# Optimization experiments

Hardware: AMD Instinct MI355X
Metric: run time of the kernel (lower is better)

Reference implementation:

```python
import jax, jax.numpy as jnp
import numpy as np

N = 400000   # active voxels
C = 64       # channels
G = 128      # voxel grid side
K = 27       # 3x3x3 kernel offsets
EPS = 1e-5   # BatchNorm eps


def _build_kernel_maps(rng):
    # random sparse 3D coordinates (unique voxels in a G^3 grid)
    lin = rng.choice(G ** 3, size=N, replace=False)
    coords = np.stack(np.unravel_index(lin, (G, G, G)), -1).astype(np.int64)  # [N,3]
    lut = np.full(G ** 3, N, dtype=np.int32)  # sentinel N = missing neighbor
    lut[lin] = np.arange(N, dtype=np.int32)
    offs = np.stack(np.meshgrid([-1, 0, 1], [-1, 0, 1], [-1, 0, 1], indexing='ij'), -1).reshape(-1, 3)  # [27,3]
    nbr = np.full((3, K, N), N, dtype=np.int32)
    for di, d in enumerate((1, 2, 3)):
        for k in range(K):
            nc = coords + offs[k] * d
            valid = np.all((nc >= 0) & (nc < G), axis=1)
            idx = np.ravel_multi_index(nc[valid].T, (G, G, G))
            nbr[di, k, valid] = lut[idx]
    return nbr


def setup_inputs() -> dict:
    key = jax.random.key(0)
    ks = jax.random.split(key, 20)
    rng = np.random.default_rng(0)
    nbr = jnp.asarray(_build_kernel_maps(rng))  # [3,27,N] int32
    s = 0.05
    inp = {
        'feats': jax.random.normal(ks[0], (N, C), jnp.float32),
        'nbr': nbr,
        # conv_init (dilation 1) + its BN
        'W_init': jax.random.normal(ks[1], (K, C, C), jnp.float32) * s,
        'b_init': jax.random.normal(ks[2], (C,), jnp.float32) * s,
        'g_init': jnp.ones((C,), jnp.float32),
        'be_init': jnp.zeros((C,), jnp.float32),
        'm_init': jax.random.normal(ks[3], (C,), jnp.float32) * s,
        'v_init': jax.random.uniform(ks[4], (C,), jnp.float32, 0.5, 1.5),
        # three branches (dilations 1,2,3), stacked on leading axis
        'W_br': jax.random.normal(ks[5], (3, K, C, C), jnp.float32) * s,
        'b_br': jax.random.normal(ks[6], (3, C), jnp.float32) * s,
        'g_br': jnp.ones((3, C), jnp.float32),
        'be_br': jnp.zeros((3, C), jnp.float32),
        'm_br': jax.random.normal(ks[7], (3, C), jnp.float32) * s,
        'v_br': jax.random.uniform(ks[8], (3, C), jnp.float32, 0.5, 1.5),
        # conv_out: 1x1 conv C -> 1
        'W_out': jax.random.normal(ks[9], (C, 1), jnp.float32) * s,
        'b_out': jax.random.normal(ks[10], (1,), jnp.float32) * s,
    }
    return inp


def _sparse_conv3(feats, nbr_k, W, b):
    # feats [N,C], nbr_k [27,N] (index N = missing), W [27,C,Cout], b [Cout]
    fpad = jnp.concatenate([feats, jnp.zeros((1, feats.shape[1]), feats.dtype)], 0)
    def step(acc, wn):
        Wk, nk = wn
        return acc + fpad[nk] @ Wk, None
    init = jnp.zeros((feats.shape[0], W.shape[-1]), feats.dtype) + b
    out, _ = jax.lax.scan(step, init, (W, nbr_k))
    return out


def _bn_relu(x, g, b, m, v):
    # inference-mode BatchNorm followed by ReLU
    return jax.nn.relu((x - m) * (g * jax.lax.rsqrt(v + EPS)) + b)


def reference(feats, nbr, W_init, b_init, g_init, be_init, m_init, v_init,
              W_br, b_br, g_br, be_br, m_br, v_br, W_out, b_out):
    x_init = _bn_relu(_sparse_conv3(feats, nbr[0], W_init, b_init),
                      g_init, be_init, m_init, v_init)
    def branch(W, b, g, be, m, v, nb):
        return _bn_relu(_sparse_conv3(x_init, nb, W, b), g, be, m, v)
    xb = jax.vmap(branch)(W_br, b_br, g_br, be_br, m_br, v_br, nbr)  # [3,N,C]
    x_fused = xb.sum(0) + x_init
    att = jax.nn.sigmoid(x_fused @ W_out + b_out)  # [N,1]
    return att
```

## Files before the change

kernel.cpp:

```cpp
#include <hip/hip_runtime.h>
#include <hip/hip_bf16.h>
#include <math.h>

#define NV 400000
#define ROWS_BLK 192
#define GRID_CONV 2084

typedef __bf16 bfv8 __attribute__((ext_vector_type(8)));
typedef float f32x4 __attribute__((ext_vector_type(4)));

#define GLOAD_LDS16(gp, lp) __builtin_amdgcn_global_load_lds(                 \
    (const __attribute__((address_space(1))) void*)(gp),                     \
    (__attribute__((address_space(3))) void*)(lp), 16, 0, 0)

__global__ void prep_feats_k(const float* __restrict__ feats,
                             __bf16* __restrict__ fpad,
                             __bf16* __restrict__ xpad)
{
    long t = (long)blockIdx.x * blockDim.x + threadIdx.x;
    long base = t * 4;
    const long nfeat = (long)NV * 64;
    const long total = (long)(NV + 1) * 64;
    if (base < total) {
        float x0 = 0.f, x1 = 0.f, x2 = 0.f, x3 = 0.f;
        if (base < nfeat) {
            const float4 v = *(const float4*)(feats + base);
            x0 = v.x; x1 = v.y; x2 = v.z; x3 = v.w;
        }
        union { __bf16 b[4]; ushort4 u; } pk;
        pk.b[0] = (__bf16)x0; pk.b[1] = (__bf16)x1;
        pk.b[2] = (__bf16)x2; pk.b[3] = (__bf16)x3;
        *(ushort4*)(fpad + base) = pk.u;
    }
    if (t < 64) xpad[(long)NV * 64 + t] = (__bf16)0.f;
}

__global__ void prep_w_k(const float* __restrict__ Winit,
                         const float* __restrict__ Wbr,
                         __bf16* __restrict__ wpk)
{
    int e = blockIdx.x * 256 + threadIdx.x;
    int i  = e & 7;
    int l  = (e >> 3) & 63;
    int cb = (e >> 9) & 3;
    int kc = (e >> 11) & 1;
    int kk = e >> 12;
    int k  = kk % 27;
    int s  = kk / 27;
    int cin  = kc * 32 + (l >> 4) * 8 + i;
    int cout = cb * 16 + (l & 15);
    float v = (s == 0) ? Winit[(k * 64 + cin) * 64 + cout]
                       : Wbr[(((s - 1) * 27 + k) * 64 + cin) * 64 + cout];
    wpk[e] = (__bf16)v;
}

__global__ void prep_bn_k(const float* __restrict__ b_init, const float* __restrict__ g_init,
                          const float* __restrict__ be_init, const float* __restrict__ m_init,
                          const float* __restrict__ v_init,
                          const float* __restrict__ b_br, const float* __restrict__ g_br,
                          const float* __restrict__ be_br, const float* __restrict__ m_br,
                          const float* __restrict__ v_br,
                          float* __restrict__ scale, float* __restrict__ shiftb)
{
    int t = threadIdx.x;
    int s = t >> 6, c = t & 63;
    float g, be, m, v, b;
    if (s == 0) { g = g_init[c]; be = be_init[c]; m = m_init[c]; v = v_init[c]; b = b_init[c]; }
    else { int o = (s - 1) * 64 + c; g = g_br[o]; be = be_br[o]; m = m_br[o]; v = v_br[o]; b = b_br[o]; }
    float sc = g / sqrtf(v + 1e-5f);
    scale[t]  = sc;
    shiftb[t] = (b - m) * sc + be;
}

struct Idx3 { int v[3]; };

__device__ __forceinline__ Idx3 load_idx3(const int* __restrict__ nbr_t,
                                          long base, int l15)
{
    Idx3 r;
#pragma unroll
    for (int rg = 0; rg < 3; rg++) {
        long rr = base + rg * 16 + l15;
        rr = (rr < NV) ? rr : (NV - 1);
        r.v[rg] = nbr_t[rr];
    }
    return r;
}

__device__ __forceinline__ void stage_b(const __bf16* __restrict__ wtap,
                                        __bf16* lds_dst, int wid, int lane)
{
#pragma unroll
    for (int j = 0; j < 2; j++) {
        int chunk = wid * 2 + j;
        const __bf16* gp = wtap + chunk * 512 + lane * 8;
        __bf16* lp = lds_dst + chunk * 512;
        GLOAD_LDS16(gp, lp);
    }
}

__device__ __forceinline__ void issue_A3(const __bf16* __restrict__ src,
                                         const Idx3 idx, int lg,
                                         bfv8 a0[3], bfv8 a1[3])
{
#pragma unroll
    for (int rg = 0; rg < 3; rg++) {
        const bfv8* ar = (const bfv8*)(src + (size_t)idx.v[rg] * 64);
        a0[rg] = ar[lg];
        a1[rg] = ar[4 + lg];
    }
}

__device__ __forceinline__ void mfma_tap3(const __bf16* bbuf, int lane,
                                          const bfv8 a0[3], const bfv8 a1[3],
                                          f32x4 acc[3][4])
{
    const bfv8* wp = (const bfv8*)bbuf;
#pragma unroll
    for (int cb = 0; cb < 4; cb++) {
        bfv8 b0 = wp[cb * 64 + lane];
#pragma unroll
        for (int rg = 0; rg < 3; rg++)
            acc[rg][cb] = __builtin_amdgcn_mfma_f32_16x16x32_bf16(a0[rg], b0, acc[rg][cb], 0, 0, 0);
    }
#pragma unroll
    for (int cb = 0; cb < 4; cb++) {
        bfv8 b1 = wp[(4 + cb) * 64 + lane];
#pragma unroll
        for (int rg = 0; rg < 3; rg++)
            acc[rg][cb] = __builtin_amdgcn_mfma_f32_16x16x32_bf16(a1[rg], b1, acc[rg][cb], 0, 0, 0);
    }
}


__global__ __launch_bounds__(256, 4)
void conv_init_k(const __bf16* __restrict__ fpad, const int* __restrict__ nbr,
                 const __bf16* __restrict__ wpk, const float* __restrict__ scale,
                 const float* __restrict__ shiftb, const float* __restrict__ wout,
                 __bf16* __restrict__ xpad, float* __restrict__ logitpart)
{
    __shared__ __bf16 smem[4 * 4096];
    __bf16* tile = smem;
    const int tid = threadIdx.x;
    const int wid = tid >> 6, lane = tid & 63;
    const int l15 = lane & 15, lg = lane >> 4;
    const long base = (long)blockIdx.x * ROWS_BLK + wid * 48;

    f32x4 acc[3][4];
    f32x4 z = {0.f, 0.f, 0.f, 0.f};
#pragma unroll
    for (int a = 0; a < 3; a++)
#pragma unroll
        for (int b = 0; b < 4; b++) acc[a][b] = z;

    stage_b(wpk,                    smem + 0 * 4096, wid, lane);
    stage_b(wpk + (size_t)1 * 4096, smem + 1 * 4096, wid, lane);
    Idx3 iA = load_idx3(nbr,                  base, l15);
    Idx3 iB = load_idx3(nbr + (size_t)1 * NV, base, l15);
    __syncthreads();

    bfv8 a0[3], a1[3];
    for (int k = 0; k < 27; k++) {
        issue_A3(fpad, iA, lg, a0, a1);
        int ts = (k + 2 < 27) ? (k + 2) : 26;
        stage_b(wpk + (size_t)ts * 4096, smem + ((k + 2) & 3) * 4096, wid, lane);
        Idx3 inew = load_idx3(nbr + (size_t)ts * NV, base, l15);
        __builtin_amdgcn_s_setprio(1);
        mfma_tap3(smem + (k & 3) * 4096, lane, a0, a1, acc);
        __builtin_amdgcn_s_setprio(0);
        iA = iB; iB = inew;
        asm volatile("s_waitcnt vmcnt(5)" ::: "memory");
        __builtin_amdgcn_s_barrier();
    }

    float sc[4], sh[4], wo[4];
#pragma unroll
    for (int cb = 0; cb < 4; cb++) {
        int col = cb * 16 + l15;
        sc[cb] = scale[col]; sh[cb] = shiftb[col]; wo[cb] = wout[col];
    }
    float lacc[3][4];
#pragma unroll
    for (int rg = 0; rg < 3; rg++)
#pragma unroll
        for (int j = 0; j < 4; j++) lacc[rg][j] = 0.f;

    __syncthreads();
#pragma unroll
    for (int rg = 0; rg < 3; rg++)
#pragma unroll
        for (int cb = 0; cb < 4; cb++)
#pragma unroll
            for (int j = 0; j < 4; j++) {
                float y = fmaxf(acc[rg][cb][j] * sc[cb] + sh[cb], 0.f);
                lacc[rg][j] += y * wo[cb];
                tile[(wid * 48 + rg * 16 + lg * 4 + j) * 64 + cb * 16 + l15] = (__bf16)y;
            }
    __syncthreads();

    for (int c = tid; c < 384; c += 256) {
        int r = c >> 1, h = c & 1;
        long grow = (long)blockIdx.x * ROWS_BLK + r;
        if (grow < NV) {
            const f32x4* srcp = (const f32x4*)(tile + r * 64 + h * 32);
            f32x4* dst = (f32x4*)(xpad + grow * 64 + h * 32);
#pragma unroll
            for (int q = 0; q < 4; q++) dst[q] = srcp[q];
        }
    }

#pragma unroll
    for (int rg = 0; rg < 3; rg++) {
        float red[4];
#pragma unroll
        for (int j = 0; j < 4; j++) {
            float t = lacc[rg][j];
            t += __shfl_xor(t, 1, 64);
            t += __shfl_xor(t, 2, 64);
            t += __shfl_xor(t, 4, 64);
            t += __shfl_xor(t, 8, 64);
            red[j] = t;
        }
        if (l15 == 0) {
            long row = base + rg * 16 + lg * 4;
            if (row < NV) {
                float4 o; o.x = red[0]; o.y = red[1]; o.z = red[2]; o.w = red[3];
                *(float4*)(logitpart + row) = o;
            }
        }
    }
}

__global__ __launch_bounds__(256, 4)
void conv_br_k(const __bf16* __restrict__ xpad, const int* __restrict__ nbr,
               const __bf16* __restrict__ wpk, const float* __restrict__ scale,
               const float* __restrict__ shiftb, const float* __restrict__ wout,
               const float* __restrict__ bout, const float* __restrict__ logitpart,
               float* __restrict__ att)
{
    __shared__ __bf16 bbuf[4][4096];
    const int tid = threadIdx.x;
    const int wid = tid >> 6, lane = tid & 63;
    const int l15 = lane & 15, lg = lane >> 4;
    const long base = (long)blockIdx.x * ROWS_BLK + wid * 48;

    float wo[4];
#pragma unroll
    for (int cb = 0; cb < 4; cb++) wo[cb] = wout[cb * 16 + l15];

    float lacc[3][4];
#pragma unroll
    for (int rg = 0; rg < 3; rg++)
#pragma unroll
        for (int j = 0; j < 4; j++) lacc[rg][j] = 0.f;

    f32x4 acc[3][4];
    f32x4 z = {0.f, 0.f, 0.f, 0.f};
#pragma unroll
    for (int a = 0; a < 3; a++)
#pragma unroll
        for (int b = 0; b < 4; b++) acc[a][b] = z;

    auto do_epi = [&](int d) {
        float sc[4], sh[4];
#pragma unroll
        for (int cb = 0; cb < 4; cb++) {
            int col = (d + 1) * 64 + cb * 16 + l15;
            sc[cb] = scale[col]; sh[cb] = shiftb[col];
        }
#pragma unroll
        for (int rg = 0; rg < 3; rg++)
#pragma unroll
            for (int cb = 0; cb < 4; cb++)
#pragma unroll
                for (int j = 0; j < 4; j++) {
                    float y = fmaxf(acc[rg][cb][j] * sc[cb] + sh[cb], 0.f);
                    lacc[rg][j] += y * wo[cb];
                }
#pragma unroll
        for (int a = 0; a < 3; a++)
#pragma unroll
            for (int b = 0; b < 4; b++) acc[a][b] = z;
    };

    stage_b(wpk + (size_t)27 * 4096, bbuf[0], wid, lane);
    stage_b(wpk + (size_t)28 * 4096, bbuf[1], wid, lane);
    Idx3 iA = load_idx3(nbr,                  base, l15);
    Idx3 iB = load_idx3(nbr + (size_t)1 * NV, base, l15);
    __syncthreads();

    bfv8 a0[3], a1[3];
    for (int k = 0; k < 81; k++) {
        issue_A3(xpad, iA, lg, a0, a1);
        int ts = (k + 2 < 81) ? (k + 2) : 80;
        stage_b(wpk + (size_t)(ts + 27) * 4096, bbuf[(k + 2) & 3], wid, lane);
        Idx3 inew = load_idx3(nbr + (size_t)ts * NV, base, l15);
        __builtin_amdgcn_s_setprio(1);
        mfma_tap3(bbuf[k & 3], lane, a0, a1, acc);
        __builtin_amdgcn_s_setprio(0);
        if (k == 26 || k == 53) do_epi(k / 27);
        iA = iB; iB = inew;
        asm volatile("s_waitcnt vmcnt(5)" ::: "memory");
        __builtin_amdgcn_s_barrier();
    }
    do_epi(2);

    float bo = bout[0];
#pragma unroll
    for (int rg = 0; rg < 3; rg++) {
        float red[4];
#pragma unroll
        for (int j = 0; j < 4; j++) {
            float t = lacc[rg][j];
            t += __shfl_xor(t, 1, 64);
            t += __shfl_xor(t, 2, 64);
            t += __shfl_xor(t, 4, 64);
            t += __shfl_xor(t, 8, 64);
            red[j] = t;
        }
        if (l15 == 0) {
            long row = base + rg * 16 + lg * 4;
            if (row < NV) {
                float4 lp = *(const float4*)(logitpart + row);
                float4 o;
                o.x = 1.f / (1.f + expf(-(red[0] + lp.x + bo)));
                o.y = 1.f / (1.f + expf(-(red[1] + lp.y + bo)));
                o.z = 1.f / (1.f + expf(-(red[2] + lp.z + bo)));
                o.w = 1.f / (1.f + expf(-(red[3] + lp.w + bo)));
                *(float4*)(att + row) = o;
            }
        }
    }
}

extern "C" void kernel_launch(void* const* d_in, const int* in_sizes, int n_in,
                              void* d_out, int out_size, void* d_ws, size_t ws_size,
                              hipStream_t stream)
{
    const float* feats  = (const float*)d_in[0];
    const int*   nbr    = (const int*)d_in[1];
    const float* W_init = (const float*)d_in[2];
    const float* b_init = (const float*)d_in[3];
    const float* g_init = (const float*)d_in[4];
    const float* be_init= (const float*)d_in[5];
    const float* m_init = (const float*)d_in[6];
    const float* v_init = (const float*)d_in[7];
    const float* W_br   = (const float*)d_in[8];
    const float* b_br   = (const float*)d_in[9];
    const float* g_br   = (const float*)d_in[10];
    const float* be_br  = (const float*)d_in[11];
    const float* m_br   = (const float*)d_in[12];
    const float* v_br   = (const float*)d_in[13];
    const float* W_out  = (const float*)d_in[14];
    const float* b_out  = (const float*)d_in[15];
    float* att = (float*)d_out;

    char* ws = (char*)d_ws;
    size_t off = 0;
    auto take = [&](size_t bytes) -> char* {
        char* p = ws + off;
        off = (off + bytes + 255) & ~(size_t)255;
        return p;
    };
    __bf16* fpad      = (__bf16*)take((size_t)(NV + 1) * 64 * 2);
    __bf16* xpad      = (__bf16*)take((size_t)(NV + 1) * 64 * 2);
    __bf16* wpk       = (__bf16*)take((size_t)4 * 27 * 4096 * 2);
    float*  scale     = (float*)take(4 * 64 * 4);
    float*  shiftb    = (float*)take(4 * 64 * 4);
    float*  logitpart = (float*)take((size_t)NV * 4);
    (void)in_sizes; (void)n_in; (void)out_size; (void)ws_size;

    prep_feats_k<<<25001, 256, 0, stream>>>(feats, fpad, xpad);
    prep_w_k<<<1728, 256, 0, stream>>>(W_init, W_br, wpk);
    prep_bn_k<<<1, 256, 0, stream>>>(b_init, g_init, be_init, m_init, v_init,
                                     b_br, g_br, be_br, m_br, v_br, scale, shiftb);
    conv_init_k<<<GRID_CONV, 256, 0, stream>>>(fpad, nbr, wpk, scale, shiftb,
                                               W_out, xpad, logitpart);
    conv_br_k<<<GRID_CONV, 256, 0, stream>>>(xpad, nbr, wpk, scale, shiftb,
                                             W_out, b_out, logitpart, att);
}
```

Measured before the change: 509.6 us.

## Double-buffer gathered A fragments one tap ahead in sparse conv kernels

Both conv kernels now prefetch the gathered feature rows for the next tap into a second register set while the MFMAs for the current tap run. Neighbor indices are loaded three taps ahead instead of two. The waitcnt and barrier move to before the MFMA so that only the current A and B data must have arrived. The extra registers lower launch_bounds occupancy from 4 to 3 blocks per SM, trading latency hiding through occupancy for latency hiding through software pipelining.

```diff
diff --git a/kernel.cpp b/kernel.cpp
--- a/kernel.cpp
+++ b/kernel.cpp
@@ -133,7 +133,7 @@
 }
 
 
-__global__ __launch_bounds__(256, 4)
+__global__ __launch_bounds__(256, 3)
 void conv_init_k(const __bf16* __restrict__ fpad, const int* __restrict__ nbr,
                  const __bf16* __restrict__ wpk, const float* __restrict__ scale,
                  const float* __restrict__ shiftb, const float* __restrict__ wout,
@@ -155,22 +155,28 @@
 
     stage_b(wpk,                    smem + 0 * 4096, wid, lane);
     stage_b(wpk + (size_t)1 * 4096, smem + 1 * 4096, wid, lane);
-    Idx3 iA = load_idx3(nbr,                  base, l15);
-    Idx3 iB = load_idx3(nbr + (size_t)1 * NV, base, l15);
+    Idx3 i0 = load_idx3(nbr,                  base, l15);
+    Idx3 i1 = load_idx3(nbr + (size_t)1 * NV, base, l15);
+    Idx3 i2 = load_idx3(nbr + (size_t)2 * NV, base, l15);
     __syncthreads();
 
-    bfv8 a0[3], a1[3];
+    bfv8 aC0[3], aC1[3], aN0[3], aN1[3];
+    issue_A3(fpad, i0, lg, aC0, aC1);
+
     for (int k = 0; k < 27; k++) {
-        issue_A3(fpad, iA, lg, a0, a1);
+        issue_A3(fpad, i1, lg, aN0, aN1);
         int ts = (k + 2 < 27) ? (k + 2) : 26;
         stage_b(wpk + (size_t)ts * 4096, smem + ((k + 2) & 3) * 4096, wid, lane);
-        Idx3 inew = load_idx3(nbr + (size_t)ts * NV, base, l15);
+        int tn = (k + 3 < 27) ? (k + 3) : 26;
+        Idx3 inew = load_idx3(nbr + (size_t)tn * NV, base, l15);
+        asm volatile("s_waitcnt vmcnt(11)" ::: "memory");
+        __builtin_amdgcn_s_barrier();
         __builtin_amdgcn_s_setprio(1);
-        mfma_tap3(smem + (k & 3) * 4096, lane, a0, a1, acc);
+        mfma_tap3(smem + (k & 3) * 4096, lane, aC0, aC1, acc);
         __builtin_amdgcn_s_setprio(0);
-        iA = iB; iB = inew;
-        asm volatile("s_waitcnt vmcnt(5)" ::: "memory");
-        __builtin_amdgcn_s_barrier();
+#pragma unroll
+        for (int rg = 0; rg < 3; rg++) { aC0[rg] = aN0[rg]; aC1[rg] = aN1[rg]; }
+        i1 = i2; i2 = inew;
     }
 
     float sc[4], sh[4], wo[4];
@@ -231,7 +237,7 @@
     }
 }
 
-__global__ __launch_bounds__(256, 4)
+__global__ __launch_bounds__(256, 3)
 void conv_br_k(const __bf16* __restrict__ xpad, const int* __restrict__ nbr,
                const __bf16* __restrict__ wpk, const float* __restrict__ scale,
                const float* __restrict__ shiftb, const float* __restrict__ wout,
@@ -285,23 +291,29 @@
 
     stage_b(wpk + (size_t)27 * 4096, bbuf[0], wid, lane);
     stage_b(wpk + (size_t)28 * 4096, bbuf[1], wid, lane);
-    Idx3 iA = load_idx3(nbr,                  base, l15);
-    Idx3 iB = load_idx3(nbr + (size_t)1 * NV, base, l15);
+    Idx3 i0 = load_idx3(nbr,                  base, l15);
+    Idx3 i1 = load_idx3(nbr + (size_t)1 * NV, base, l15);
+    Idx3 i2 = load_idx3(nbr + (size_t)2 * NV, base, l15);
     __syncthreads();
 
-    bfv8 a0[3], a1[3];
+    bfv8 aC0[3], aC1[3], aN0[3], aN1[3];
+    issue_A3(xpad, i0, lg, aC0, aC1);
+
     for (int k = 0; k < 81; k++) {
-        issue_A3(xpad, iA, lg, a0, a1);
+        issue_A3(xpad, i1, lg, aN0, aN1);
         int ts = (k + 2 < 81) ? (k + 2) : 80;
         stage_b(wpk + (size_t)(ts + 27) * 4096, bbuf[(k + 2) & 3], wid, lane);
-        Idx3 inew = load_idx3(nbr + (size_t)ts * NV, base, l15);
+        int tn = (k + 3 < 81) ? (k + 3) : 80;
+        Idx3 inew = load_idx3(nbr + (size_t)tn * NV, base, l15);
+        asm volatile("s_waitcnt vmcnt(11)" ::: "memory");
+        __builtin_amdgcn_s_barrier();
         __builtin_amdgcn_s_setprio(1);
-        mfma_tap3(bbuf[k & 3], lane, a0, a1, acc);
+        mfma_tap3(bbuf[k & 3], lane, aC0, aC1, acc);
         __builtin_amdgcn_s_setprio(0);
         if (k == 26 || k == 53) do_epi(k / 27);
-        iA = iB; iB = inew;
-        asm volatile("s_waitcnt vmcnt(5)" ::: "memory");
-        __builtin_amdgcn_s_barrier();
+#pragma unroll
+        for (int rg = 0; rg < 3; rg++) { aC0[rg] = aN0[rg]; aC1[rg] = aN1[rg]; }
+        i1 = i2; i2 = inew;
     }
     do_epi(2);
 
```

Result: slower. 539.8 us (+5.9%).
